# Performance work log

Measured on AMD Instinct MI355X. Metric: run time of the kernel, lower is better.

The kernel has to match this reference:

```python
import jax, jax.numpy as jnp
import numpy as np

B, S, V, E, HL = 64, 30, 5000, 300, 256
TWOH = 2 * HL
KB, MAPD, MEMD, MLP, NCLS = 512, 512, 512, 1024, 32
L, T, NMOD, NOPS = 8, 9, 9, 6
IH, IW, CIN = 15, 10, 512 + 128


def setup_inputs():
    key = jax.random.key(0)
    ks = iter(jax.random.split(key, 64))
    g = lambda shape, s=0.05: jax.random.normal(next(ks), shape, jnp.float32) * s
    inp = {}
    inp['image'] = g((B, CIN, IH, IW), 1.0)
    inp['ques'] = jax.random.randint(next(ks), (B, S), 0, V)
    ql = jnp.sort(jax.random.randint(next(ks), (B,), 1, S + 1))[::-1]
    inp['q_len'] = ql.at[0].set(S)
    inp['embed_W'] = g((V, E))
    for d in ('f', 'b'):
        inp['lstm_Wi_' + d] = g((E, 4 * HL))
        inp['lstm_Wh_' + d] = g((HL, 4 * HL))
        inp['lstm_b_' + d] = jnp.zeros((4 * HL,), jnp.float32)
    inp['W1'] = g((T, TWOH, TWOH))
    inp['b_1'] = jnp.zeros((TWOH,), jnp.float32)
    inp['W2_w'] = g((2 * TWOH, TWOH)); inp['W2_b'] = jnp.zeros((TWOH,), jnp.float32)
    inp['W3'] = g((TWOH,))
    inp['c_0'] = g((TWOH,), 1.0)
    inp['Wmod'] = g((TWOH, NMOD))
    inp['ic1_w'] = g((KB, CIN)); inp['ic1_b'] = g((KB,), 1.0)
    inp['ic2_w'] = g((KB, KB)); inp['ic2_b'] = g((KB,), 1.0)
    inp['i2m_w'] = g((MAPD, KB)); inp['i2m_b'] = g((MAPD,), 1.0)
    inp['t2m_w'] = g((TWOH, MAPD)); inp['t2m_b'] = jnp.zeros((MAPD,), jnp.float32)
    inp['cell3_ow'] = g((4, NOPS), 1.0)
    inp['cell3_cw'] = g((4, MAPD)); inp['cell3_cb'] = jnp.zeros((4,), jnp.float32)
    inp['cell4_ow'] = g((2, NOPS), 1.0)
    inp['cell4_cw'] = g((2, MAPD)); inp['cell4_cb'] = jnp.zeros((2,), jnp.float32)
    inp['ans_ow'] = g((2, NOPS), 1.0)
    inp['ans_W'] = g((2, 2 * MAPD, MEMD)); inp['ans_b'] = jnp.zeros((2, MEMD), jnp.float32)
    inp['out1_w'] = g((TWOH + MEMD, MLP)); inp['out1_b'] = jnp.zeros((MLP,), jnp.float32)
    inp['out2_w'] = g((MLP, NCLS)); inp['out2_b'] = jnp.zeros((NCLS,), jnp.float32)
    return inp


def _conv1x1(x, w, b):
    return jnp.einsum('bchw,oc->bohw', x, w) + b[None, :, None, None]


def _lstm_dir(xW, Wh, mask, reverse):
    # xW: [S,B,4H], mask: [S,B,1] ; torch LSTM gate order i,f,g,o
    Bn, Hn = xW.shape[1], Wh.shape[0]
    def step(carry, inp):
        h, c = carry
        xw, m = inp
        z = xw + h @ Wh
        i, f, gg, o = jnp.split(z, 4, axis=-1)
        cn = jax.nn.sigmoid(f) * c + jax.nn.sigmoid(i) * jnp.tanh(gg)
        hn = jax.nn.sigmoid(o) * jnp.tanh(cn)
        return (jnp.where(m, hn, h), jnp.where(m, cn, c)), jnp.where(m, hn, 0.0)
    init = (jnp.zeros((Bn, Hn), xW.dtype), jnp.zeros((Bn, Hn), xW.dtype))
    (hF, _), outs = jax.lax.scan(step, init, (xW, mask), reverse=reverse)
    return hF, outs


def _mix3(ow, x, a, t):
    # soft op mixing (DARTS-style) for 3-input cells: x [B,D,H,W], a [B,H,W], t [B,D]
    w = jax.nn.softmax(ow)
    a4 = a[:, None]; t4 = t[:, :, None, None]
    ops = (x * t4, x + t4, x * a4, x * t4 * a4, x, a4 * t4)
    return jax.nn.elu(sum(w[k] * ops[k] for k in range(NOPS)))


def _mix4(ow, x, a1, a2, t):
    w = jax.nn.softmax(ow)
    a14 = a1[:, None]; a24 = a2[:, None]; t4 = t[:, :, None, None]
    ops = (x * t4, x + t4, x * a14, x * a24, x * a14 * a24, x * t4 * (a14 + a24))
    return jax.nn.elu(sum(w[k] * ops[k] for k in range(NOPS)))


def _forward(image, ques, q_len, embed_W, lstm_Wi_f, lstm_Wh_f, lstm_b_f, lstm_Wi_b, lstm_Wh_b, lstm_b_b, W1, b_1, W2_w, W2_b, W3, c_0, Wmod, ic1_w, ic1_b, ic2_w, ic2_b, i2m_w, i2m_b, t2m_w, t2m_b, cell3_ow, cell3_cw, cell3_cb, cell4_ow, cell4_cw, cell4_cb, ans_ow, ans_W, ans_b, out1_w, out1_b, out2_w, out2_b):
    # img_conv (1x1 conv -> ELU -> 1x1 conv)
    x = jax.nn.elu(_conv1x1(image, ic1_w, ic1_b))
    x = _conv1x1(x, ic2_w, ic2_b)
    Bn, _, Hh, Ww = x.shape
    Sn = ques.shape[1]
    # bi-LSTM over the (packed, i.e. masked) question
    emb = embed_W[ques]                                   # [B,S,E]
    mask = (jnp.arange(Sn)[None, :] < q_len[:, None])     # [B,S]
    mT = mask.T[:, :, None].astype(x.dtype) > 0           # [S,B,1] bool
    xWf = (emb @ lstm_Wi_f + lstm_b_f).transpose(1, 0, 2)
    xWb = (emb @ lstm_Wi_b + lstm_b_b).transpose(1, 0, 2)
    hF, oF = _lstm_dir(xWf, lstm_Wh_f, mT, False)
    hB, oB = _lstm_dir(xWb, lstm_Wh_b, mT, True)
    lstm_out = jnp.concatenate([oF, oB], -1).transpose(1, 0, 2)  # [B,S,2H], zero at pads
    q = jnp.concatenate([hF, hB], -1)                            # [B,2H]
    img_map = _conv1x1(x, i2m_w, i2m_b)                          # [B,MAP,H,W]
    stack = jnp.zeros((Bn, Hh, Ww, L), x.dtype)
    p = jnp.zeros((Bn, L), x.dtype).at[:, 0].set(1.0)
    mem = jnp.zeros((Bn, MEMD), x.dtype)
    c_prev = jnp.tile(c_0[None], (Bn, 1))
    e0 = jnp.zeros((L,), x.dtype).at[0].set(1.0)
    imp_loss = jnp.float32(0.0)
    read = lambda st, pp: jnp.einsum('bhwl,bl->bhw', st, pp)
    dec = lambda pp: jnp.concatenate([pp[:, 1:], jnp.zeros_like(pp[:, :1])], 1) + pp * e0
    for t in range(T):
        u = jnp.concatenate([q @ W1[t] + b_1, c_prev], 1) @ W2_w + W2_b  # [B,2H]
        wl = u @ Wmod                                                     # [B,9]
        ls = jax.nn.log_softmax(wl, axis=1)
        imp_loss = imp_loss - jnp.sum(jnp.exp(ls) * ls)
        w = jnp.exp(ls)
        attn = jax.nn.softmax(jnp.einsum('bsh,h->bs', lstm_out * u[:, None, :], W3), axis=1)
        c = jnp.einsum('bs,bsh->bh', attn, lstm_out)
        c_prev = c
        tmap = c @ t2m_w + t2m_b
        stacks, ps = [], []
        a_top = read(stack, p)     # attention at stack top
        # modules 0-3: overwrite at current pointer (pointer shift is commented out in source)
        for m in range(4):
            out = jnp.einsum('bdhw,d->bhw', _mix3(cell3_ow[m], img_map, a_top, tmap), cell3_cw[m]) + cell3_cb[m]
            pb = p[:, None, None, :]
            stacks.append(stack * (1.0 - pb) + out[..., None] * pb)
            ps.append(p)
        # modules 4-5: pop one (soft pointer decrement), then write
        p_dec = dec(p)
        a2 = read(stack, p_dec)
        for m in range(2):
            out = jnp.einsum('bdhw,d->bhw', _mix4(cell4_ow[m], img_map, a_top, a2, tmap), cell4_cw[m]) + cell4_cb[m]
            pb = p_dec[:, None, None, :]
            stacks.append(stack * (1.0 - pb) + out[..., None] * pb)
            ps.append(p_dec)
        # modules 6-7: answer cells -> memory update, stack untouched
        pooled6 = jnp.mean(_mix3(ans_ow[0], img_map, a_top, tmap), axis=(2, 3))
        mem6 = jnp.concatenate([pooled6, tmap], 1) @ ans_W[0] + ans_b[0]
        stacks.append(stack); ps.append(p)
        pooled7 = jnp.mean(_mix4(ans_ow[1], img_map, a_top, a2, tmap), axis=(2, 3))
        mem7 = jnp.concatenate([pooled7, tmap], 1) @ ans_W[1] + ans_b[1]
        stacks.append(stack); ps.append(p_dec)
        # module 8: NoOp
        stacks.append(stack); ps.append(p)
        # soft mixing over modules (the scatter-heavy part)
        stack = jnp.einsum('bm,bmhwl->bhwl', w, jnp.stack(stacks, 1))
        p = jnp.einsum('bm,bml->bl', w, jnp.stack(ps, 1))
        mem = w[:, 6:7] * mem6 + w[:, 7:8] * mem7 + (1.0 - w[:, 6:7] - w[:, 7:8]) * mem
    h1 = jax.nn.elu(jnp.concatenate([q, mem], 1) @ out1_w + out1_b)
    logits = h1 @ out2_w + out2_b
    return logits, imp_loss


def reference(image, ques, q_len, embed_W, lstm_Wi_f, lstm_Wh_f, lstm_b_f, lstm_Wi_b, lstm_Wh_b, lstm_b_b, W1, b_1, W2_w, W2_b, W3, c_0, Wmod, ic1_w, ic1_b, ic2_w, ic2_b, i2m_w, i2m_b, t2m_w, t2m_b, cell3_ow, cell3_cw, cell3_cb, cell4_ow, cell4_cw, cell4_cb, ans_ow, ans_W, ans_b, out1_w, out1_b, out2_w, out2_b):
    return _forward(image, ques, q_len, embed_W, lstm_Wi_f, lstm_Wh_f, lstm_b_f, lstm_Wi_b, lstm_Wh_b, lstm_b_b, W1, b_1, W2_w, W2_b, W3, c_0, Wmod, ic1_w, ic1_b, ic2_w, ic2_b, i2m_w, i2m_b, t2m_w, t2m_b, cell3_ow, cell3_cw, cell3_cb, cell4_ow, cell4_cw, cell4_cb, ans_ow, ans_W, ans_b, out1_w, out1_b, out2_w, out2_b)
```

## Files before the change

kernel.cpp:

```cpp
#include <hip/hip_runtime.h>
#include <hip/hip_fp16.h>
#include <math.h>

#define DEV __device__ __forceinline__

DEV float fexp(float x){ return __expf(x); }
DEV float elu_(float x){ return x > 0.f ? x : fexp(x) - 1.f; }
DEV float sigm_(float x){ return 1.f/(1.f + fexp(-x)); }
DEV float tanh_(float x){ float e = fexp(2.f*x); return 1.f - 2.f/(e + 1.f); }
DEV unsigned bf16r(float x){ unsigned u = __float_as_uint(x);
  return (u + 0x7fffu + ((u>>16)&1u)) >> 16; }
DEV float blo(unsigned u){ return __uint_as_float(u << 16); }
DEV float bhi(unsigned u){ return __uint_as_float(u & 0xffff0000u); }
DEV float bl(unsigned short u){ return __uint_as_float(((unsigned)u) << 16); }

using frag  = __attribute__((ext_vector_type(8))) short;
using fragh = __attribute__((ext_vector_type(8))) _Float16;
using f32x4 = __attribute__((ext_vector_type(4))) float;

DEV uint4 cload16w(const void* p){
  uint4 r;
  asm volatile("global_load_dwordx4 %0, %1, off sc0 sc1\n\ts_waitcnt vmcnt(0)"
               : "=v"(r) : "v"(p) : "memory");
  return r;
}
DEV uint4 cload16nw(const void* p){
  uint4 r;
  asm volatile("global_load_dwordx4 %0, %1, off sc0 sc1"
               : "=v"(r) : "v"(p) : "memory");
  return r;
}

DEV void d_packB(const float* __restrict__ W, short* __restrict__ Bp,
                 int KC, int Ng, int Ksrc, int N, int trans, int idx)
{
  if (idx >= KC*Ng*64) return;
  int lane = idx & 63;
  int g    = (idx >> 6) % Ng;
  int kc   = idx / (64*Ng);
  int n = g*16 + (lane & 15);
  int kb = kc*32 + ((lane >> 4) << 3);
  unsigned o[4];
#pragma unroll
  for (int jj = 0; jj < 4; ++jj) {
    int k0 = kb + 2*jj;
    float v0 = (k0   < Ksrc) ? (trans ? W[(size_t)n*Ksrc + k0]   : W[(size_t)(k0)*N + n])   : 0.f;
    float v1 = (k0+1 < Ksrc) ? (trans ? W[(size_t)n*Ksrc + k0+1] : W[(size_t)(k0+1)*N + n]) : 0.f;
    o[jj] = bf16r(v0) | (bf16r(v1) << 16);
  }
  *(uint4*)(Bp + (size_t)idx*8) = make_uint4(o[0], o[1], o[2], o[3]);
}

DEV void d_packImg(const float* __restrict__ image, short* __restrict__ Ap, int idx)
{
  int lane = idx & 63;
  int kc   = (idx >> 6) % 20;
  int mt   = idx / 1280;
  int row = mt*16 + (lane & 15);
  int b = row / 150, p = row % 150;
  int cb = kc*32 + ((lane >> 4) << 3);
  unsigned o[4];
#pragma unroll
  for (int jj = 0; jj < 4; ++jj) {
    float v0 = image[((size_t)b*640 + cb + 2*jj    )*150 + p];
    float v1 = image[((size_t)b*640 + cb + 2*jj + 1)*150 + p];
    o[jj] = bf16r(v0) | (bf16r(v1) << 16);
  }
  *(uint4*)(Ap + (size_t)idx*8) = make_uint4(o[0], o[1], o[2], o[3]);
}

DEV void d_packEmb(const float* __restrict__ embedW, const int* __restrict__ ques,
                   short* __restrict__ Ap, int idx)
{
  int lane = idx & 63;
  int kc   = (idx >> 6) % 10;
  int mt   = idx / 640;
  int row = mt*16 + (lane & 15);
  int q = ques[row];
  int kb = kc*32 + ((lane >> 4) << 3);
  unsigned o[4];
#pragma unroll
  for (int jj = 0; jj < 4; ++jj) {
    int k0 = kb + 2*jj;
    float v0 = (k0   < 300) ? embedW[(size_t)q*300 + k0]   : 0.f;
    float v1 = (k0+1 < 300) ? embedW[(size_t)q*300 + k0+1] : 0.f;
    o[jj] = bf16r(v0) | (bf16r(v1) << 16);
  }
  *(uint4*)(Ap + (size_t)idx*8) = make_uint4(o[0], o[1], o[2], o[3]);
}

__global__ __launch_bounds__(256)
void megapack_k(const float* __restrict__ c0, const float* __restrict__ c3ow,
                const float* __restrict__ c4ow, const float* __restrict__ aow,
                float* __restrict__ stack, float* __restrict__ pvecA,
                float* __restrict__ mem, float* __restrict__ cprev,
                float* __restrict__ swb, float* __restrict__ pl,
                const float* __restrict__ Whf, const float* __restrict__ Whb,
                unsigned* __restrict__ whT,
                float* __restrict__ hbufz, int* __restrict__ flagz,
                const float* __restrict__ ic1w, short* __restrict__ w1p,
                const float* __restrict__ ic2w, short* __restrict__ w2mp,
                const float* __restrict__ i2mw, short* __restrict__ w3mp,
                const float* __restrict__ Wif, short* __restrict__ wifp,
                const float* __restrict__ Wib, short* __restrict__ wibp,
                const float* __restrict__ image, short* __restrict__ imgP,
                const float* __restrict__ embedW, const int* __restrict__ ques,
                short* __restrict__ embp,
                const float* __restrict__ t2mw, unsigned* __restrict__ t2pp,
                const float* __restrict__ W2w, unsigned short* __restrict__ w2bp,
                const float* __restrict__ ansW, unsigned short* __restrict__ answp)
{
  const int bx = blockIdx.x, tid = threadIdx.x;
  if (bx < 320) {
    int idx = bx*256 + tid;
    int stride = 320*256;
    for (int i = idx; i < 64*150*8; i += stride) stack[i] = 0.f;
    for (int i = idx; i < 64*8;    i += stride) pvecA[i] = ((i & 7) == 0) ? 1.f : 0.f;
    for (int i = idx; i < 64*512;  i += stride) mem[i] = 0.f;
    for (int i = idx; i < 64*512;  i += stride) cprev[i] = c0[i & 511];
    for (int i = idx; i < 9*2*64*512; i += stride) pl[i] = 0.f;
    for (int i = idx; i < 32768;   i += stride) hbufz[i] = 0.f;
    if (idx < 256) flagz[idx] = 0;
    if (idx < 8) {
      const float* ow = (idx < 4) ? (c3ow + idx*6)
                      : (idx < 6) ? (c4ow + (idx-4)*6)
                                  : (aow  + (idx-6)*6);
      float mx = ow[0];
      for (int m = 1; m < 6; ++m) mx = fmaxf(mx, ow[m]);
      float e[6]; float s = 0.f;
      for (int m = 0; m < 6; ++m) { e[m] = fexp(ow[m]-mx); s += e[m]; }
      for (int m = 0; m < 6; ++m) swb[idx*6+m] = e[m]/s;
    }
  } else if (bx < 1344) {
    int idx = (bx-320)*256 + tid;
    int dd  = idx >> 17;
    int rem = idx & 131071;
    int kp  = rem >> 10;
    int zc  = rem & 1023;
    const float* Wh = dd ? Whb : Whf;
    __half2 hv = __floats2half2_rn(Wh[(size_t)(2*kp)*1024 + zc],
                                   Wh[(size_t)(2*kp+1)*1024 + zc]);
    whT[((size_t)dd << 17) + (zc << 7) + kp] = *(unsigned*)&hv;
  } else if (bx < 1504) {
    d_packB(ic1w, w1p, 20, 32, 640, 512, 1, (bx-1344)*256 + tid);
  } else if (bx < 1632) {
    d_packB(ic2w, w2mp, 16, 32, 512, 512, 1, (bx-1504)*256 + tid);
  } else if (bx < 1760) {
    d_packB(i2mw, w3mp, 16, 32, 512, 512, 1, (bx-1632)*256 + tid);
  } else if (bx < 1920) {
    d_packB(Wif, wifp, 10, 64, 300, 1024, 0, (bx-1760)*256 + tid);
  } else if (bx < 2080) {
    d_packB(Wib, wibp, 10, 64, 300, 1024, 0, (bx-1920)*256 + tid);
  } else if (bx < 5080) {
    d_packImg(image, imgP, (bx-2080)*256 + tid);
  } else if (bx < 5380) {
    d_packEmb(embedW, ques, embp, (bx-5080)*256 + tid);
  } else if (bx < 5892) {
    int idx = (bx-5380)*256 + tid;
    int k = idx >> 8, c = idx & 255;
    t2pp[idx] = bf16r(t2mw[(size_t)k*512 + c]) | (bf16r(t2mw[(size_t)k*512 + 256 + c]) << 16);
  } else if (bx < 7940) {
    int i = (bx-5892)*256 + tid;
    w2bp[i] = (unsigned short)bf16r(W2w[i]);
  } else {
    int i = (bx-7940)*256 + tid;
    answp[i] = (unsigned short)bf16r(ansW[i]);
  }
}

__global__ __launch_bounds__(256)
void gemmM_k(const short* __restrict__ ApA, const short* __restrict__ ApB,
             const short* __restrict__ BpA, const short* __restrict__ BpB,
             const float* __restrict__ biasA, const float* __restrict__ biasB,
             void* __restrict__ CoutA, void* __restrict__ CoutB,
             int KC, int Ng, int N, int mode, int act, int KCout)
{
  __shared__ float lds[4][16][68];
  const int z = blockIdx.z;
  const short* Ap = z ? ApB : ApA;
  const short* Bp = z ? BpB : BpA;
  const float* bias = z ? biasB : biasA;
  void* Cout = z ? CoutB : CoutA;
  const int tid = threadIdx.x, lane = tid & 63, w = tid >> 6;
  const int mt = blockIdx.y*4 + w;
  const int ncol0 = blockIdx.x*64;
  const short* Abase = Ap + (((size_t)mt*KC) << 9) + lane*8;
  const short* Bbase = Bp + (((size_t)blockIdx.x*4) << 9) + lane*8;
  f32x4 acc0 = {0.f,0.f,0.f,0.f}, acc1 = acc0, acc2 = acc0, acc3 = acc0;
#pragma unroll 2
  for (int kc = 0; kc < KC; ++kc) {
    frag a = *(const frag*)(Abase + ((size_t)kc << 9));
    const short* bk = Bbase + (((size_t)kc*Ng) << 9);
    frag b0 = *(const frag*)(bk);
    frag b1 = *(const frag*)(bk + 512);
    frag b2 = *(const frag*)(bk + 1024);
    frag b3 = *(const frag*)(bk + 1536);
    acc0 = __builtin_amdgcn_mfma_f32_16x16x32_bf16(a, b0, acc0, 0, 0, 0);
    acc1 = __builtin_amdgcn_mfma_f32_16x16x32_bf16(a, b1, acc1, 0, 0, 0);
    acc2 = __builtin_amdgcn_mfma_f32_16x16x32_bf16(a, b2, acc2, 0, 0, 0);
    acc3 = __builtin_amdgcn_mfma_f32_16x16x32_bf16(a, b3, acc3, 0, 0, 0);
  }
  {
    int colb = lane & 15, rowb = (lane >> 4)*4;
#pragma unroll
    for (int r = 0; r < 4; ++r) {
      lds[w][rowb+r][ 0+colb] = acc0[r];
      lds[w][rowb+r][16+colb] = acc1[r];
      lds[w][rowb+r][32+colb] = acc2[r];
      lds[w][rowb+r][48+colb] = acc3[r];
    }
  }
  __syncthreads();
  if (mode == 0) {
    float* C = (float*)Cout;
    int mloc = lane >> 2, q4 = lane & 3;
    size_t rowoff = (size_t)(mt*16 + mloc)*N + ncol0 + q4*16;
#pragma unroll
    for (int i = 0; i < 4; ++i) {
      float4 v = *(float4*)&lds[w][mloc][q4*16 + i*4];
      const float* bp = bias + ncol0 + q4*16 + i*4;
      v.x += bp[0]; v.y += bp[1]; v.z += bp[2]; v.w += bp[3];
      if (act) { v.x = elu_(v.x); v.y = elu_(v.y); v.z = elu_(v.z); v.w = elu_(v.w); }
      *(float4*)&C[rowoff + i*4] = v;
    }
  } else if (mode == 1) {
    short* C = (short*)Cout;
    int m = lane & 15, qb = (lane >> 4)*8;
#pragma unroll
    for (int h = 0; h < 2; ++h) {
      int nl = h*32 + qb;
      unsigned o[4];
#pragma unroll
      for (int jj = 0; jj < 4; ++jj) {
        float v0 = lds[w][m][nl + 2*jj]     + bias[ncol0 + nl + 2*jj];
        float v1 = lds[w][m][nl + 2*jj + 1] + bias[ncol0 + nl + 2*jj + 1];
        if (act) { v0 = elu_(v0); v1 = elu_(v1); }
        o[jj] = bf16r(v0) | (bf16r(v1) << 16);
      }
      *(uint4*)(C + (((size_t)mt*KCout + (ncol0 >> 5) + h) << 9) + lane*8)
          = make_uint4(o[0], o[1], o[2], o[3]);
    }
  } else {
    unsigned short* C = (unsigned short*)Cout;
    int row = lane >> 2, cb = (lane & 3)*16;
#pragma unroll
    for (int h = 0; h < 2; ++h) {
      unsigned o[4];
#pragma unroll
      for (int jj = 0; jj < 4; ++jj) {
        float v0 = lds[w][row][cb + h*8 + 2*jj]     + bias[ncol0 + cb + h*8 + 2*jj];
        float v1 = lds[w][row][cb + h*8 + 2*jj + 1] + bias[ncol0 + cb + h*8 + 2*jj + 1];
        if (act) { v0 = elu_(v0); v1 = elu_(v1); }
        o[jj] = bf16r(v0) | (bf16r(v1) << 16);
      }
      *(uint4*)&C[(size_t)(mt*16 + row)*N + ncol0 + cb + h*8]
          = make_uint4(o[0], o[1], o[2], o[3]);
    }
  }
}

__global__ __launch_bounds__(512)
void gemm64b_k(const float* __restrict__ A1, long zA1, int K1log,
               const float* __restrict__ A2, int K2,
               const float* __restrict__ B, long zB,
               const float* __restrict__ bias, int zbias,
               float* __restrict__ C, long zC, int N, int act)
{
  const int K1 = 1 << K1log;
  const int Kt = K1 + K2;
  __shared__ __align__(16) float As[8][1024];
  __shared__ float part[8][8][64];
  const int tid = threadIdx.x;
  const int z = blockIdx.z;
  const int r0 = blockIdx.y*8;
  {
    const float* a1 = A1 + (size_t)z*zA1;
    const int nf4 = (8*K1) >> 2;
    for (int e4 = tid; e4 < nf4; e4 += 512) {
      int r = e4 >> (K1log-2);
      int k4 = (e4 & ((K1>>2)-1)) << 2;
      *(float4*)&As[r][k4] = *(const float4*)&a1[(size_t)(r0+r)*K1 + k4];
    }
    if (K2 > 0) {
      for (int e4 = tid; e4 < 1024; e4 += 512) {
        int r = e4 >> 7;
        int k4 = (e4 & 127) << 2;
        *(float4*)&As[r][K1+k4] = *(const float4*)&A2[(size_t)(r0+r)*512 + k4];
      }
    }
  }
  __syncthreads();
  const int lane = tid & 63, w = tid >> 6;
  const int n = blockIdx.x*64 + lane;
  const bool nv = n < N;
  const int kseg = Kt >> 3;
  const int k0 = w*kseg;
  const float* Bp = B + (size_t)z*zB + (size_t)k0*N + (nv ? n : 0);
  float acc[8] = {0,0,0,0,0,0,0,0};
#pragma unroll 8
  for (int kk = 0; kk < kseg; ++kk) {
    float bv = nv ? Bp[(size_t)kk*N] : 0.f;
    int k = k0 + kk;
#pragma unroll
    for (int r = 0; r < 8; ++r) acc[r] += As[r][k]*bv;
  }
#pragma unroll
  for (int r = 0; r < 8; ++r) part[w][r][lane] = acc[r];
  __syncthreads();
  {
    int r = tid >> 6, c = tid & 63;
    int nn = blockIdx.x*64 + c;
    if (nn < N) {
      float s = 0.f;
#pragma unroll
      for (int w2 = 0; w2 < 8; ++w2) s += part[w2][r][c];
      s += bias ? bias[(size_t)z*zbias + nn] : 0.f;
      if (act == 1) s = elu_(s);
      C[(size_t)z*zC + (size_t)(r0+r)*N + nn] = s;
    }
  }
}

__global__ __launch_bounds__(256)
void lstmM_k(const float* __restrict__ xWf, const float* __restrict__ xWb,
             const unsigned* __restrict__ whT, const int* __restrict__ qlen,
             unsigned long long* __restrict__ hbuf, int* __restrict__ flags,
             float* __restrict__ lstm_out, float* __restrict__ qout)
{
  const int bx = blockIdx.x;
  const int d = bx & 1, g = (bx >> 1) & 3, n = bx >> 3;
  const int tid = threadIdx.x, lane = tid & 63, w = tid >> 6;
  const int q = lane >> 4, cl = lane & 15;
  __shared__ __align__(16) unsigned short Wl[65536];

#pragma unroll 4
  for (int rb = 0; rb < 32; ++rb) {
    int lcrow = rb*8 + (tid >> 5);
    int gt = lcrow >> 6, c = lcrow & 63;
    int zc = gt*256 + n*64 + c;
    uint4 v = *(const uint4*)(whT + (((size_t)d*1024 + zc) << 7) + ((tid & 31) << 2));
    int byteoff = (lcrow << 9) + ((((tid & 31) << 4)) ^ ((lcrow & 7) << 4));
    *(uint4*)((char*)Wl + byteoff) = v;
  }

  const float* xW = d ? xWb : xWf;
  const int b   = g*16 + cl;
  const int c4  = w*16 + q*4;
  const int hc4 = n*64 + c4;
  const int len = qlen[b];
  float cst[4] = {0.f,0.f,0.f,0.f}, hst[4] = {0.f,0.f,0.f,0.f};
  int* flg = flags + ((d*4 + g) << 2);
  const int bofs = (cl & 7) << 4;
  __syncthreads();

  for (int ss = 0; ss < 30; ++ss) {
    const int s = d ? (29 - ss) : ss;
    const float* xr = xW + (size_t)b*30720 + (size_t)s*1024 + hc4;
    f32x4 xwv[4];
#pragma unroll
    for (int gt = 0; gt < 4; ++gt) xwv[gt] = *(const f32x4*)(xr + gt*256);

    if (ss > 0) {
      for (;;) {
        uint4 f4 = cload16w(flg);
        if ((int)f4.x >= ss && (int)f4.y >= ss &&
            (int)f4.z >= ss && (int)f4.w >= ss) break;
      }
      __builtin_amdgcn_sched_barrier(0);
    }
    const char* hbr = (const char*)(hbuf + ((size_t)(((ss & 1)*2 + d)*4 + g) << 9))
                    + (cl << 9) + (q << 4);
    union { uint4 u; fragh f; } hv[8];
#pragma unroll
    for (int ks = 0; ks < 8; ++ks) hv[ks].u = cload16nw(hbr + (ks << 6));
    asm volatile("s_waitcnt vmcnt(0)" ::: "memory");
    __builtin_amdgcn_sched_barrier(0);

    f32x4 acc0 = {0.f,0.f,0.f,0.f}, acc1 = acc0, acc2 = acc0, acc3 = acc0;
#pragma unroll
    for (int ks = 0; ks < 8; ++ks) {
      const int kb = ((ks << 6) + (q << 4)) ^ bofs;
      const char* wb = (const char*)Wl + ((w*16 + cl) << 9) + kb;
      fragh a0 = *(const fragh*)(wb);
      fragh a1 = *(const fragh*)(wb + (64 << 9));
      fragh a2 = *(const fragh*)(wb + (128 << 9));
      fragh a3 = *(const fragh*)(wb + (192 << 9));
      acc0 = __builtin_amdgcn_mfma_f32_16x16x32_f16(a0, hv[ks].f, acc0, 0, 0, 0);
      acc1 = __builtin_amdgcn_mfma_f32_16x16x32_f16(a1, hv[ks].f, acc1, 0, 0, 0);
      acc2 = __builtin_amdgcn_mfma_f32_16x16x32_f16(a2, hv[ks].f, acc2, 0, 0, 0);
      acc3 = __builtin_amdgcn_mfma_f32_16x16x32_f16(a3, hv[ks].f, acc3, 0, 0, 0);
    }
    const bool m = s < len;
    f32x4 lo4;
    float hvv[4];
#pragma unroll
    for (int r = 0; r < 4; ++r) {
      float iv = acc0[r] + xwv[0][r];
      float fv = acc1[r] + xwv[1][r];
      float gv = acc2[r] + xwv[2][r];
      float o_ = acc3[r] + xwv[3][r];
      float cn = sigm_(fv)*cst[r] + sigm_(iv)*tanh_(gv);
      float hn = sigm_(o_)*tanh_(cn);
      float hk = m ? hn : hst[r];
      cst[r] = m ? cn : cst[r];
      hst[r] = hk;
      hvv[r] = hk;
      lo4[r] = m ? hn : 0.f;
    }
    unsigned long long* hbw = hbuf + ((size_t)((((ss & 1) ^ 1)*2 + d)*4 + g) << 9);
    union { unsigned long long u; __half2 h2[2]; } hp;
    hp.h2[0] = __floats2half2_rn(hvv[0], hvv[1]);
    hp.h2[1] = __floats2half2_rn(hvv[2], hvv[3]);
    __hip_atomic_store(hbw + cl*64 + (hc4 >> 2), hp.u,
                       __ATOMIC_RELAXED, __HIP_MEMORY_SCOPE_AGENT);
    *(f32x4*)(lstm_out + (((size_t)b*30 + s) << 9) + (d << 8) + hc4) = lo4;
    asm volatile("s_waitcnt vmcnt(0)" ::: "memory");
    __syncthreads();
    if (tid == 0)
      __hip_atomic_store(&flg[n], ss + 1, __ATOMIC_RELAXED, __HIP_MEMORY_SCOPE_AGENT);
  }
  *(f32x4*)(qout + ((size_t)b << 9) + (d << 8) + hc4) =
      f32x4{hst[0], hst[1], hst[2], hst[3]};
}

__global__ __launch_bounds__(1024)
void kcattn3_k(const float* __restrict__ tmp1, const float* __restrict__ cprevB,
               const unsigned short* __restrict__ w2bp, const float* __restrict__ W2b,
               const float* __restrict__ Wmod,
               const float* __restrict__ lstm_out, const float* __restrict__ W3,
               const unsigned* __restrict__ t2pp, const float* __restrict__ t2mb,
               float* __restrict__ woutAll, float* __restrict__ imp_part,
               float* __restrict__ cout, float* __restrict__ tmapv, int t)
{
  int b = blockIdx.x;
  int tid = threadIdx.x;
  int lane = tid & 63, wave = tid >> 6;
  __shared__ float A2s[1024];
  __shared__ float ush[512];
  __shared__ float upart[512];
  __shared__ float sC[512];
  __shared__ float cpart[512];
  __shared__ float tpart[4][512];
  __shared__ float wl[9];
  __shared__ float sc[32], at[32];
  if (tid < 512) A2s[tid] = tmp1[b*512 + tid];
  else           A2s[tid] = cprevB[b*512 + (tid - 512)];
  __syncthreads();
  {
    int col = tid & 511, kh = tid >> 9;
    const unsigned short* wp = w2bp + ((size_t)kh*512)*512 + col;
    const float* av = A2s + kh*512;
    float acc = 0.f;
#pragma unroll 8
    for (int k = 0; k < 512; ++k) acc += av[k]*bl(wp[(size_t)k*512]);
    if (kh) upart[col] = acc;
    __syncthreads();
    if (!kh) ush[col] = acc + upart[col] + W2b[col];
  }
  __syncthreads();
  for (int s = wave; s < 30; s += 16) {
    float acc = 0.f;
    const float* lo = lstm_out + ((size_t)b*30 + s)*512;
#pragma unroll
    for (int h = lane; h < 512; h += 64) acc += lo[h]*ush[h]*W3[h];
#pragma unroll
    for (int off = 32; off; off >>= 1) acc += __shfl_down(acc, off);
    if (lane == 0) sc[s] = acc;
  }
  if (wave < 9) {
    float acc = 0.f;
#pragma unroll
    for (int k = lane; k < 512; k += 64) acc += ush[k]*Wmod[k*9+wave];
#pragma unroll
    for (int off = 32; off; off >>= 1) acc += __shfl_down(acc, off);
    if (lane == 0) wl[wave] = acc;
  }
  __syncthreads();
  if (tid == 0) {
    float mx = wl[0];
    for (int m = 1; m < 9; ++m) mx = fmaxf(mx, wl[m]);
    float s = 0.f;
    for (int m = 0; m < 9; ++m) s += fexp(wl[m]-mx);
    float ls = logf(s);
    float ent = 0.f;
    for (int m = 0; m < 9; ++m) {
      float l = wl[m]-mx-ls;
      float w = fexp(l);
      woutAll[t*576 + b*9 + m] = w;
      ent -= w*l;
    }
    imp_part[t*64+b] = ent;
  }
  if (wave == 1) {
    float v = (lane < 30) ? sc[lane] : -3.4e38f;
    float mx = v;
#pragma unroll
    for (int off = 32; off; off >>= 1) mx = fmaxf(mx, __shfl_xor(mx, off));
    float e = (lane < 30) ? fexp(v-mx) : 0.f;
    float ssum = e;
#pragma unroll
    for (int off = 32; off; off >>= 1) ssum += __shfl_xor(ssum, off);
    if (lane < 30) at[lane] = e/ssum;
  }
  __syncthreads();
  {
    int h = tid & 511, seg = tid >> 9;
    float acc = 0.f;
    int s0 = seg ? 15 : 0, s1 = seg ? 30 : 15;
    for (int s = s0; s < s1; ++s) acc += at[s]*lstm_out[((size_t)b*30 + s)*512 + h];
    if (seg) cpart[h] = acc;
    __syncthreads();
    if (!seg) {
      float tot = acc + cpart[h];
      cout[b*512+h] = tot;
      sC[h] = tot;
    }
  }
  __syncthreads();
  {
    int c2 = tid & 255, ks = tid >> 8;
    float a0 = 0.f, a1 = 0.f;
    const unsigned* tp = t2pp + c2;
#pragma unroll 8
    for (int k = ks*128; k < ks*128 + 128; ++k) {
      float cv = sC[k];
      unsigned wv2 = tp[(size_t)k*256];
      a0 += cv*blo(wv2);
      a1 += cv*bhi(wv2);
    }
    tpart[ks][c2]       = a0;
    tpart[ks][256 + c2] = a1;
  }
  __syncthreads();
  if (tid < 512) {
    float v = tpart[0][tid] + tpart[1][tid] + tpart[2][tid] + tpart[3][tid];
    tmapv[b*512 + tid] = v + t2mb[tid];
  }
}

__global__ __launch_bounds__(256)
void modules2_k(const unsigned short* __restrict__ imapB, const float* __restrict__ tmapv,
                float* __restrict__ stack, const float* __restrict__ pvecIn,
                float* __restrict__ pvecOut,
                const float* __restrict__ swb, const float* __restrict__ c3w,
                const float* __restrict__ c3b, const float* __restrict__ c4w,
                const float* __restrict__ c4b, const float* __restrict__ wmod,
                float* __restrict__ plt)
{
  int b  = blockIdx.x;
  int pb = blockIdx.y;
  int lane = threadIdx.x & 63, wave = threadIdx.x >> 6;
  __shared__ float sT[512];
  __shared__ float pv[8], pd[8], wm[9];
  __shared__ float wpart[4][2][512];
  for (int j = threadIdx.x; j < 512; j += 256) sT[j] = tmapv[b*512 + j];
  if (threadIdx.x < 8) pv[threadIdx.x] = pvecIn[b*8+threadIdx.x];
  if (threadIdx.x >= 64 && threadIdx.x < 73) wm[threadIdx.x-64] = wmod[b*9 + threadIdx.x-64];
  __syncthreads();
  if (threadIdx.x < 8) {
    int l = threadIdx.x;
    pd[l] = (l < 7 ? pv[l+1] : 0.f) + (l == 0 ? pv[0] : 0.f);
  }
  __syncthreads();
  if (pb == 0 && threadIdx.x < 8) {
    int l = threadIdx.x;
    float WP = wm[0]+wm[1]+wm[2]+wm[3] + wm[6] + wm[8];
    float WD = wm[4]+wm[5] + wm[7];
    pvecOut[b*8+l] = WP*pv[l] + WD*pd[l];
  }

  float W[8][6];
#pragma unroll
  for (int m = 0; m < 8; ++m)
#pragma unroll
    for (int i = 0; i < 6; ++i) W[m][i] = swb[m*6+i];
  float W03 = wm[0]+wm[1]+wm[2]+wm[3];
  float W45 = wm[4]+wm[5];

  float acc6[8], acc7[8];
#pragma unroll
  for (int i = 0; i < 8; ++i) { acc6[i] = 0.f; acc7[i] = 0.f; }

  for (int pi = 0; pi < 2; ++pi) {
    int p = pb*8 + wave*2 + pi;
    if (p < 150) {
      const float* st = stack + ((size_t)b*150 + p)*8;
      float a = 0.f, av2 = 0.f;
#pragma unroll
      for (int l = 0; l < 8; ++l) { float v = st[l]; a += v*pv[l]; av2 += v*pd[l]; }
      float part[6] = {0,0,0,0,0,0};
#pragma unroll 2
      for (int i = 0; i < 8; ++i) {
        int d = i*64 + lane;
        float x = bl(imapB[((size_t)b*150 + p)*512 + d]);
        float t = sT[d];
#pragma unroll
        for (int m = 0; m < 4; ++m) {
          float c1 = W[m][0]*t + W[m][1] + W[m][4] + (W[m][2] + W[m][3]*t)*a;
          float c0 = W[m][1]*t + W[m][5]*t*a;
          part[m] += elu_(c1*x + c0) * c3w[m*512+d];
        }
#pragma unroll
        for (int m = 0; m < 2; ++m) {
          float c1 = W[4+m][0]*t + W[4+m][1] + W[4+m][2]*a + W[4+m][3]*av2
                   + W[4+m][4]*a*av2 + W[4+m][5]*t*(a+av2);
          part[4+m] += elu_(c1*x + W[4+m][1]*t) * c4w[m*512+d];
        }
        float c16 = W[6][0]*t + W[6][1] + W[6][4] + (W[6][2] + W[6][3]*t)*a;
        float c06 = W[6][1]*t + W[6][5]*t*a;
        acc6[i] += elu_(c16*x + c06);
        float c17 = W[7][0]*t + W[7][1] + W[7][2]*a + W[7][3]*av2
                  + W[7][4]*a*av2 + W[7][5]*t*(a+av2);
        acc7[i] += elu_(c17*x + W[7][1]*t);
      }
#pragma unroll
      for (int m = 0; m < 6; ++m) {
#pragma unroll
        for (int off = 32; off; off >>= 1) part[m] += __shfl_down(part[m], off);
        part[m] = __shfl(part[m], 0);
      }
      float r3  = wm[0]*(part[0]+c3b[0]) + wm[1]*(part[1]+c3b[1])
                + wm[2]*(part[2]+c3b[2]) + wm[3]*(part[3]+c3b[3]);
      float r45 = wm[4]*(part[4]+c4b[0]) + wm[5]*(part[5]+c4b[1]);
      if (lane < 8) {
        int l = lane;
        size_t idx = ((size_t)b*150 + p)*8 + l;
        stack[idx] = stack[idx]*(1.f - W03*pv[l] - W45*pd[l])
                   + pv[l]*r3 + pd[l]*r45;
      }
    }
  }
#pragma unroll
  for (int i = 0; i < 8; ++i) {
    wpart[wave][0][i*64+lane] = acc6[i];
    wpart[wave][1][i*64+lane] = acc7[i];
  }
  __syncthreads();
  for (int e = threadIdx.x; e < 1024; e += 256) {
    int which = e >> 9, d = e & 511;
    float s = wpart[0][which][d] + wpart[1][which][d]
            + wpart[2][which][d] + wpart[3][which][d];
    atomicAdd(&plt[(size_t)which*32768 + b*512 + d], s * (1.f/150.f));
  }
}

__global__ __launch_bounds__(512)
void ansall_k(const float* __restrict__ plt, const float* __restrict__ tmapv,
              const unsigned short* __restrict__ answp, const float* __restrict__ ansb,
              float* __restrict__ m67o)
{
  const int z = blockIdx.z;
  const int t = z >> 1, zz = z & 1;
  __shared__ __align__(16) float As[8][1024];
  __shared__ float part[8][8][64];
  const int tid = threadIdx.x;
  const int r0 = blockIdx.y*8;
  const int nc0 = blockIdx.x*64;
  const int lane = tid & 63, w = tid >> 6;

  for (int e4 = tid; e4 < 1024; e4 += 512) {
    int r = e4 >> 7, k4 = (e4 & 127) << 2;
    *(float4*)&As[r][k4]     = *(const float4*)&plt[(size_t)z*32768 + (size_t)(r0+r)*512 + k4];
    *(float4*)&As[r][512+k4] = *(const float4*)&tmapv[(size_t)t*32768 + (size_t)(r0+r)*512 + k4];
  }
  __syncthreads();
  {
    const unsigned short* Bp = answp + (size_t)zz*524288
                             + (size_t)(w*128)*512 + nc0 + lane;
    float acc[8] = {0,0,0,0,0,0,0,0};
    int k0 = w*128;
#pragma unroll 8
    for (int kk = 0; kk < 128; ++kk) {
      float bv = bl(Bp[(size_t)kk*512]);
#pragma unroll
      for (int r = 0; r < 8; ++r) acc[r] += As[r][k0+kk]*bv;
    }
#pragma unroll
    for (int r = 0; r < 8; ++r) part[w][r][lane] = acc[r];
  }
  __syncthreads();
  {
    int r = tid >> 6, c = tid & 63;
    float s = 0.f;
#pragma unroll
    for (int w2 = 0; w2 < 8; ++w2) s += part[w2][r][c];
    m67o[(size_t)z*32768 + (size_t)(r0+r)*512 + nc0 + c] = s + ansb[zz*512 + nc0 + c];
  }
}

__global__ __launch_bounds__(512)
void memfin_k(const float* __restrict__ woutAll, const float* __restrict__ m67t,
              float* __restrict__ memb)
{
  int b = blockIdx.x;
  int tid = threadIdx.x;
  __shared__ float w6s[9], w7s[9], coef[9];
  if (tid < 9)       w6s[tid] = woutAll[tid*576 + b*9 + 6];
  else if (tid < 18) w7s[tid-9] = woutAll[(tid-9)*576 + b*9 + 7];
  __syncthreads();
  if (tid == 0) {
    float c = 1.f;
    for (int t = 8; t >= 0; --t) { coef[t] = c; c *= (1.f - w6s[t] - w7s[t]); }
  }
  __syncthreads();
  float acc = 0.f;
#pragma unroll
  for (int t = 0; t < 9; ++t) {
    float m6 = m67t[(((size_t)t*2 + 0)*64 + b)*512 + tid];
    float m7 = m67t[(((size_t)t*2 + 1)*64 + b)*512 + tid];
    acc += coef[t]*(w6s[t]*m6 + w7s[t]*m7);
  }
  memb[b*512 + tid] = acc;
}

__global__ __launch_bounds__(256)
void imp_k(const float* __restrict__ part, float* __restrict__ out)
{
  int lane = threadIdx.x & 63, wave = threadIdx.x >> 6;
  float acc = 0.f;
  for (int i = threadIdx.x; i < 576; i += 256) acc += part[i];
#pragma unroll
  for (int off = 32; off; off >>= 1) acc += __shfl_down(acc, off);
  __shared__ float red[4];
  if (lane == 0) red[wave] = acc;
  __syncthreads();
  if (threadIdx.x == 0) out[0] = red[0]+red[1]+red[2]+red[3];
}

extern "C" void kernel_launch(void* const* d_in, const int* in_sizes, int n_in,
                              void* d_out, int out_size, void* d_ws, size_t ws_size,
                              hipStream_t stream)
{
  (void)in_sizes; (void)n_in; (void)out_size; (void)ws_size;
  const float* image = (const float*)d_in[0];
  const int*   ques  = (const int*)d_in[1];
  const int*   qlen  = (const int*)d_in[2];
  const float* embedW= (const float*)d_in[3];
  const float* Wi_f  = (const float*)d_in[4];
  const float* Wh_f  = (const float*)d_in[5];
  const float* b_f   = (const float*)d_in[6];
  const float* Wi_b  = (const float*)d_in[7];
  const float* Wh_b  = (const float*)d_in[8];
  const float* b_b   = (const float*)d_in[9];
  const float* W1    = (const float*)d_in[10];
  const float* b1    = (const float*)d_in[11];
  const float* W2w   = (const float*)d_in[12];
  const float* W2b   = (const float*)d_in[13];
  const float* W3    = (const float*)d_in[14];
  const float* c0    = (const float*)d_in[15];
  const float* Wmod  = (const float*)d_in[16];
  const float* ic1w  = (const float*)d_in[17];
  const float* ic1b  = (const float*)d_in[18];
  const float* ic2w  = (const float*)d_in[19];
  const float* ic2b  = (const float*)d_in[20];
  const float* i2mw  = (const float*)d_in[21];
  const float* i2mb  = (const float*)d_in[22];
  const float* t2mw  = (const float*)d_in[23];
  const float* t2mb  = (const float*)d_in[24];
  const float* c3ow  = (const float*)d_in[25];
  const float* c3cw  = (const float*)d_in[26];
  const float* c3cb  = (const float*)d_in[27];
  const float* c4ow  = (const float*)d_in[28];
  const float* c4cw  = (const float*)d_in[29];
  const float* c4cb  = (const float*)d_in[30];
  const float* aow   = (const float*)d_in[31];
  const float* ansW  = (const float*)d_in[32];
  const float* ansb  = (const float*)d_in[33];
  const float* o1w   = (const float*)d_in[34];
  const float* o1b   = (const float*)d_in[35];
  const float* o2w   = (const float*)d_in[36];
  const float* o2b   = (const float*)d_in[37];
  float* out = (float*)d_out;
  float* ws  = (float*)d_ws;

  size_t off = 0;
  auto alloc = [&](size_t n){ float* p = ws + off; off += n; return p; };
  short* imgP  = (short*)alloc(600ull*20*64*8/2);
  short* X1p   = (short*)alloc(600ull*16*64*8/2);
  short* X2p   = (short*)alloc(600ull*16*64*8/2);
  short* w1p   = (short*)alloc(20*32*64*8/2);
  short* w2mp  = (short*)alloc(16*32*64*8/2);
  short* w3mp  = (short*)alloc(16*32*64*8/2);
  short* wifp  = (short*)alloc(10*64*64*8/2);
  short* wibp  = (short*)alloc(10*64*64*8/2);
  short* embp  = (short*)alloc(120ull*10*64*8/2);
  unsigned short* imapB = (unsigned short*)alloc(9600ull*512/2);
  unsigned* t2pp = (unsigned*)alloc(512*256);
  unsigned short* w2bp  = (unsigned short*)alloc(524288/2);
  unsigned short* answp = (unsigned short*)alloc(1048576/2);
  float* xWfb  = alloc(64ull*30*1024);
  float* xWbb  = alloc(64ull*30*1024);
  float* lout  = alloc(64ull*30*512);
  float* qbuf  = alloc(64*512);
  float* stck  = alloc(64*150*8);
  float* pvecA = alloc(64*8);
  float* pvecB = alloc(64*8);
  float* memb  = alloc(64*512);
  float* cprev = alloc(64*512);
  float* tmp1a = alloc(9ull*64*512);
  float* wmwA  = alloc(9*64*9);
  float* impp  = alloc(9*64);
  float* swb   = alloc(48);
  float* pl    = alloc(9ull*2*64*512);
  float* m67t  = alloc(9ull*2*64*512);
  float* tmapv = alloc(9ull*64*512);
  float* h1b   = alloc(64*1024);
  unsigned* whT = (unsigned*)alloc(2ull*1024*128);
  float* hbufW  = alloc(32768);
  int*   flagsI = (int*)alloc(256);

  megapack_k<<<12036, 256, 0, stream>>>(
      c0, c3ow, c4ow, aow, stck, pvecA, memb, cprev, swb, pl,
      Wh_f, Wh_b, whT, hbufW, flagsI,
      ic1w, w1p, ic2w, w2mp, i2mw, w3mp, Wi_f, wifp, Wi_b, wibp,
      image, imgP, embedW, ques, embp, t2mw, t2pp,
      W2w, w2bp, ansW, answp);

  gemmM_k<<<dim3(8,150,1), 256, 0, stream>>>(imgP, imgP, w1p, w1p, ic1b, ic1b,
                                             X1p, X1p, 20, 32, 512, 1, 1, 16);
  gemmM_k<<<dim3(8,150,1), 256, 0, stream>>>(X1p, X1p, w2mp, w2mp, ic2b, ic2b,
                                             X2p, X2p, 16, 32, 512, 1, 0, 16);
  gemmM_k<<<dim3(8,150,1), 256, 0, stream>>>(X2p, X2p, w3mp, w3mp, i2mb, i2mb,
                                             imapB, imapB, 16, 32, 512, 2, 0, 0);
  gemmM_k<<<dim3(16,30,2), 256, 0, stream>>>(embp, embp, wifp, wibp, b_f, b_b,
                                             xWfb, xWbb, 10, 64, 1024, 0, 0, 0);

  lstmM_k<<<32, 256, 0, stream>>>(xWfb, xWbb, whT, qlen,
                                  (unsigned long long*)hbufW, flagsI, lout, qbuf);

  gemm64b_k<<<dim3(8,8,9), 512, 0, stream>>>(
      qbuf, 0, 9, (const float*)nullptr, 0,
      W1, 262144, b1, 0, tmp1a, 32768, 512, 0);

  for (int t = 0; t < 9; ++t) {
    float* pvIn  = (t & 1) ? pvecB : pvecA;
    float* pvOut = (t & 1) ? pvecA : pvecB;
    kcattn3_k<<<64, 1024, 0, stream>>>(
        tmp1a + (size_t)t*32768, cprev, w2bp, W2b,
        Wmod, lout, W3, t2pp, t2mb,
        wmwA, impp, cprev, tmapv + (size_t)t*32768, t);
    modules2_k<<<dim3(64,19), 256, 0, stream>>>(
        imapB, tmapv + (size_t)t*32768, stck, pvIn, pvOut, swb,
        c3cw, c3cb, c4cw, c4cb,
        wmwA + (size_t)t*576, pl + (size_t)t*65536);
  }

  ansall_k<<<dim3(8,8,18), 512, 0, stream>>>(pl, tmapv, answp, ansb, m67t);

  memfin_k<<<64, 512, 0, stream>>>(wmwA, m67t, memb);
  gemm64b_k<<<dim3(16,8,1), 512, 0, stream>>>(
      qbuf, 0, 9, memb, 512, o1w, 0, o1b, 0, h1b, 0, 1024, 1);
  gemm64b_k<<<dim3(1,8,1), 512, 0, stream>>>(
      h1b, 0, 10, (const float*)nullptr, 0, o2w, 0, o2b, 0, out, 0, 32, 0);
  imp_k<<<1, 256, 0, stream>>>(impp, out + 2048);
}
```

Baseline: 947.7 us.

## Move W2 controller GEMM out of attention kernel into modules kernel for next step

The per-step W2 projection (concat of tmp1 and previous c times W2) is removed from the 1024-thread attention kernel. The first step is precomputed by a gemm64b launch, and each later step is computed by an extra grid row in the modules kernel during the previous iteration. Each extra block does an 8-row by 64-column tile that reuses the bf16 weights across rows. This shortens the serial critical path of the attention kernel at the cost of a larger modules grid and a dependency on cprev being written before modules runs.

```diff
diff --git a/kernel.cpp b/kernel.cpp
--- a/kernel.cpp
+++ b/kernel.cpp
@@ -424,9 +424,7 @@
 }
 
 __global__ __launch_bounds__(1024)
-void kcattn3_k(const float* __restrict__ tmp1, const float* __restrict__ cprevB,
-               const unsigned short* __restrict__ w2bp, const float* __restrict__ W2b,
-               const float* __restrict__ Wmod,
+void kcattn3_k(const float* __restrict__ u, const float* __restrict__ Wmod,
                const float* __restrict__ lstm_out, const float* __restrict__ W3,
                const unsigned* __restrict__ t2pp, const float* __restrict__ t2mb,
                float* __restrict__ woutAll, float* __restrict__ imp_part,
@@ -435,28 +433,13 @@
   int b = blockIdx.x;
   int tid = threadIdx.x;
   int lane = tid & 63, wave = tid >> 6;
-  __shared__ float A2s[1024];
   __shared__ float ush[512];
-  __shared__ float upart[512];
   __shared__ float sC[512];
   __shared__ float cpart[512];
   __shared__ float tpart[4][512];
   __shared__ float wl[9];
   __shared__ float sc[32], at[32];
-  if (tid < 512) A2s[tid] = tmp1[b*512 + tid];
-  else           A2s[tid] = cprevB[b*512 + (tid - 512)];
-  __syncthreads();
-  {
-    int col = tid & 511, kh = tid >> 9;
-    const unsigned short* wp = w2bp + ((size_t)kh*512)*512 + col;
-    const float* av = A2s + kh*512;
-    float acc = 0.f;
-#pragma unroll 8
-    for (int k = 0; k < 512; ++k) acc += av[k]*bl(wp[(size_t)k*512]);
-    if (kh) upart[col] = acc;
-    __syncthreads();
-    if (!kh) ush[col] = acc + upart[col] + W2b[col];
-  }
+  if (tid < 512) ush[tid] = u[b*512 + tid];
   __syncthreads();
   for (int s = wave; s < 30; s += 16) {
     float acc = 0.f;
@@ -539,20 +522,54 @@
 }
 
 __global__ __launch_bounds__(256)
-void modules2_k(const unsigned short* __restrict__ imapB, const float* __restrict__ tmapv,
-                float* __restrict__ stack, const float* __restrict__ pvecIn,
-                float* __restrict__ pvecOut,
-                const float* __restrict__ swb, const float* __restrict__ c3w,
-                const float* __restrict__ c3b, const float* __restrict__ c4w,
-                const float* __restrict__ c4b, const float* __restrict__ wmod,
-                float* __restrict__ plt)
-{
-  int b  = blockIdx.x;
+void modu_k(const unsigned short* __restrict__ imapB, const float* __restrict__ tmapv,
+            float* __restrict__ stack, const float* __restrict__ pvecIn,
+            float* __restrict__ pvecOut,
+            const float* __restrict__ swb, const float* __restrict__ c3w,
+            const float* __restrict__ c3b, const float* __restrict__ c4w,
+            const float* __restrict__ c4b, const float* __restrict__ wmod,
+            float* __restrict__ plt,
+            const float* __restrict__ tmp1n, const float* __restrict__ cprevB,
+            const unsigned short* __restrict__ w2bp, const float* __restrict__ W2b,
+            float* __restrict__ ubuf, int do_u)
+{
   int pb = blockIdx.y;
   int lane = threadIdx.x & 63, wave = threadIdx.x >> 6;
   __shared__ float sT[512];
   __shared__ float pv[8], pd[8], wm[9];
   __shared__ float wpart[4][2][512];
+  if (pb == 19) {
+    if (!do_u) return;
+    const int x = blockIdx.x;
+    const int r0 = (x >> 3) * 8, nc0 = (x & 7) * 64;
+    const int kg0 = wave * 256;
+    const float* src = (wave < 2) ? tmp1n : cprevB;
+    const int kb2 = (wave & 1) * 256;
+    float acc[8] = {0,0,0,0,0,0,0,0};
+    const unsigned short* Bp = w2bp + (size_t)kg0*512 + nc0 + lane;
+    const float* As0 = src + (size_t)r0*512 + kb2;
+#pragma unroll 4
+    for (int kk = 0; kk < 256; ++kk) {
+      float bv = bl(Bp[(size_t)kk*512]);
+#pragma unroll
+      for (int r = 0; r < 8; ++r) acc[r] += As0[(size_t)r*512 + kk] * bv;
+    }
+    float (*prt)[8][64] = (float(*)[8][64])wpart;
+#pragma unroll
+    for (int r = 0; r < 8; ++r) prt[wave][r][lane] = acc[r];
+    __syncthreads();
+    {
+      int r = threadIdx.x >> 6, c = lane;
+#pragma unroll
+      for (int p2 = 0; p2 < 2; ++p2) {
+        int rr = r + p2*4;
+        float s2 = prt[0][rr][c] + prt[1][rr][c] + prt[2][rr][c] + prt[3][rr][c];
+        ubuf[(size_t)(r0 + rr)*512 + nc0 + c] = s2 + W2b[nc0 + c];
+      }
+    }
+    return;
+  }
+  int b = blockIdx.x;
   for (int j = threadIdx.x; j < 512; j += 256) sT[j] = tmapv[b*512 + j];
   if (threadIdx.x < 8) pv[threadIdx.x] = pvecIn[b*8+threadIdx.x];
   if (threadIdx.x >= 64 && threadIdx.x < 73) wm[threadIdx.x-64] = wmod[b*9 + threadIdx.x-64];
@@ -798,6 +815,7 @@
   float* memb  = alloc(64*512);
   float* cprev = alloc(64*512);
   float* tmp1a = alloc(9ull*64*512);
+  float* ubuf  = alloc(64*512);
   float* wmwA  = alloc(9*64*9);
   float* impp  = alloc(9*64);
   float* swb   = alloc(48);
@@ -831,18 +849,21 @@
   gemm64b_k<<<dim3(8,8,9), 512, 0, stream>>>(
       qbuf, 0, 9, (const float*)nullptr, 0,
       W1, 262144, b1, 0, tmp1a, 32768, 512, 0);
+  gemm64b_k<<<dim3(8,8,1), 512, 0, stream>>>(
+      tmp1a, 0, 9, cprev, 512, W2w, 0, W2b, 0, ubuf, 0, 512, 0);
 
   for (int t = 0; t < 9; ++t) {
     float* pvIn  = (t & 1) ? pvecB : pvecA;
     float* pvOut = (t & 1) ? pvecA : pvecB;
-    kcattn3_k<<<64, 1024, 0, stream>>>(
-        tmp1a + (size_t)t*32768, cprev, w2bp, W2b,
-        Wmod, lout, W3, t2pp, t2mb,
-        wmwA, impp, cprev, tmapv + (size_t)t*32768, t);
-    modules2_k<<<dim3(64,19), 256, 0, stream>>>(
+    kcattn3_k<<<64, 1024, 0, stream>>>(ubuf, Wmod, lout, W3, t2pp, t2mb,
+                                       wmwA, impp, cprev,
+                                       tmapv + (size_t)t*32768, t);
+    modu_k<<<dim3(64,20), 256, 0, stream>>>(
         imapB, tmapv + (size_t)t*32768, stck, pvIn, pvOut, swb,
         c3cw, c3cb, c4cw, c4cb,
-        wmwA + (size_t)t*576, pl + (size_t)t*65536);
+        wmwA + (size_t)t*576, pl + (size_t)t*65536,
+        tmp1a + (size_t)(t < 8 ? t+1 : 0)*32768, cprev, w2bp, W2b, ubuf,
+        (t < 8) ? 1 : 0);
   }
 
   ansall_k<<<dim3(8,8,18), 512, 0, stream>>>(pl, tmapv, answp, ansb, m67t);
```

Result: faster. 904.9 us (-4.5%).
